# Optimization experiments

Hardware: AMD Instinct MI355X
Metric: run time of the kernel (lower is better)

## Reference

```python
import jax, jax.numpy as jnp
import numpy as np
from jax import lax

B, CIN, H, W = 64, 256, 56, 56
WIDTH = 64            # bottleneck width (planes * base_width/64 * groups)
COUT = 256            # planes * expansion
SP_BUDGET = 0.5       # spatial budget
CH_BUDGET = 0.5       # channel budget
K_SP = int(SP_BUDGET * H * W)    # 1568 kept pixels
K_CH = int(CH_BUDGET * WIDTH)    # 32 kept channels
EPS = 1e-5


def _conv(x, w, stride=1, pad=0):
    return lax.conv_general_dilated(
        x, w, (stride, stride), [(pad, pad), (pad, pad)],
        dimension_numbers=('NCHW', 'OIHW', 'NCHW'))


def _bn(x, g, b, m, v):
    scale = g / jnp.sqrt(v + EPS)
    return x * scale[None, :, None, None] + (b - m * scale)[None, :, None, None]


def setup_inputs() -> dict:
    key = jax.random.key(0)
    ks = jax.random.split(key, 6)
    inp = {
        'x': jax.random.normal(ks[0], (B, CIN, H, W), jnp.float32),
        'conv1_w': jax.random.normal(ks[1], (WIDTH, CIN, 1, 1), jnp.float32) * 0.05,
        'bn1_g': jnp.ones((WIDTH,), jnp.float32), 'bn1_b': jnp.zeros((WIDTH,), jnp.float32),
        'bn1_m': jnp.zeros((WIDTH,), jnp.float32), 'bn1_v': jnp.ones((WIDTH,), jnp.float32),
        'conv2_w': jax.random.normal(ks[2], (WIDTH, WIDTH, 3, 3), jnp.float32) * 0.05,
        'bn2_g': jnp.ones((WIDTH,), jnp.float32), 'bn2_b': jnp.zeros((WIDTH,), jnp.float32),
        'bn2_m': jnp.zeros((WIDTH,), jnp.float32), 'bn2_v': jnp.ones((WIDTH,), jnp.float32),
        'conv3_w': jax.random.normal(ks[3], (COUT, WIDTH, 1, 1), jnp.float32) * 0.05,
        'bn3_g': jnp.ones((COUT,), jnp.float32), 'bn3_b': jnp.zeros((COUT,), jnp.float32),
        'bn3_m': jnp.zeros((COUT,), jnp.float32), 'bn3_v': jnp.ones((COUT,), jnp.float32),
        'fc_w': jax.random.normal(ks[4], (WIDTH, CIN), jnp.float32) * 0.05,
        'fc_b': jnp.zeros((WIDTH,), jnp.float32),
        'mask_w': jax.random.normal(ks[5], (1, CIN, 1, 1), jnp.float32) * 0.05,
        'mask_b': jnp.zeros((1,), jnp.float32),
    }
    return inp


def reference(x, conv1_w, bn1_g, bn1_b, bn1_m, bn1_v,
              conv2_w, bn2_g, bn2_b, bn2_m, bn2_v,
              conv3_w, bn3_g, bn3_b, bn3_m, bn3_v,
              fc_w, fc_b, mask_w, mask_b):
    identity = x

    # --- ChannelVectorUnit: pooled fc saliency -> hard channel-budget top-k mask [B, WIDTH]
    pooled = x.mean(axis=(2, 3))                         # [B, CIN]
    ch_sal = jax.nn.sigmoid(pooled @ fc_w.T + fc_b)      # [B, WIDTH]
    ch_kth = lax.top_k(ch_sal, K_CH)[0][:, -1:]          # [B, 1]
    vector = (ch_sal >= ch_kth).astype(x.dtype)          # hard 0/1

    # --- MaskUnit: 1x1-conv spatial saliency -> hard spatial-budget top-k mask [B,1,H,W]
    sp_sal = _conv(x, mask_w) + mask_b[None, :, None, None]   # [B,1,H,W]
    sp_flat = sp_sal.reshape(B, H * W)
    sp_kth = lax.top_k(sp_flat, K_SP)[0][:, -1:]
    mask = (sp_flat >= sp_kth).astype(x.dtype).reshape(B, 1, H, W)
    # dilated mask: 3x3 max-dilation (receptive field of the 3x3 conv)
    mask_dilate = lax.reduce_window(mask, 0.0, lax.max, (1, 1, 3, 3), (1, 1, 1, 1), 'SAME')

    # --- masked bottleneck (dense compute, mask multiplies; stride = 1)
    out = _conv(x, conv1_w)
    out = jax.nn.relu(_bn(out, bn1_g, bn1_b, bn1_m, bn1_v)) * mask_dilate
    out = out * vector[:, :, None, None]                 # channel pruning
    out = _conv(out, conv2_w, stride=1, pad=1)
    out = jax.nn.relu(_bn(out, bn2_g, bn2_b, bn2_m, bn2_v)) * mask
    out = out * vector[:, :, None, None]
    out = _conv(out, conv3_w)
    out = _bn(out, bn3_g, bn3_b, bn3_m, bn3_v) * mask
    out = jax.nn.relu(identity + out)
    return out
```

## Files before the change

### kernel.cpp

```cpp
#include <hip/hip_runtime.h>
#include <math.h>

#define BATCH 64
#define CIN   256
#define HH    56
#define WW    56
#define HW    (HH*WW)
#define WIDTH 64
#define COUT  256
#define K_CH  32
#define K_SP  1568
#define EPS   1e-5f

typedef short short8 __attribute__((ext_vector_type(8)));
typedef float f32x4 __attribute__((ext_vector_type(4)));

#define MFMA16(a, b, c) __builtin_amdgcn_mfma_f32_16x16x32_bf16((a), (b), (c), 0, 0, 0)

__device__ __forceinline__ unsigned short f2bf(float f) {
    unsigned u = __builtin_bit_cast(unsigned, f);
    u += 0x7fffu + ((u >> 16) & 1u);
    return (unsigned short)(u >> 16);
}

__global__ __launch_bounds__(256) void k_poolsal(const float* __restrict__ x,
                                                 const float* __restrict__ mask_w,
                                                 double* __restrict__ pooled,
                                                 double* __restrict__ spart) {
    int ct = blockIdx.x, b = blockIdx.y;
    int tid = threadIdx.x;
    __shared__ double pl[16][257];
    double sp0[4], sp1[4], sp2[4], spt[4];
#pragma unroll
    for (int k = 0; k < 4; k++) { sp0[k] = 0.0; sp1[k] = 0.0; sp2[k] = 0.0; spt[k] = 0.0; }

#pragma clang loop unroll(disable)
    for (int c = 0; c < 16; c++) {
        const float* xr = x + ((size_t)(b * CIN + ct * 16 + c)) * HW;
        double w = (double)mask_w[ct * 16 + c];
        f32x4 v0 = *(const f32x4*)(xr + tid * 4);
        f32x4 v1 = *(const f32x4*)(xr + 1024 + tid * 4);
        f32x4 v2 = *(const f32x4*)(xr + 2048 + tid * 4);
        double s = 0.0;
#pragma unroll
        for (int k = 0; k < 4; k++) {
            double d0 = (double)v0[k], d1 = (double)v1[k], d2 = (double)v2[k];
            sp0[k] += d0 * w; sp1[k] += d1 * w; sp2[k] += d2 * w;
            s += d0 + d1 + d2;
        }
        if (tid < 16) {
            f32x4 v3 = *(const f32x4*)(xr + 3072 + tid * 4);
#pragma unroll
            for (int k = 0; k < 4; k++) {
                double d3 = (double)v3[k];
                spt[k] += d3 * w;
                s += d3;
            }
        }
        pl[c][tid] = s;
    }
    double* so = spart + ((size_t)(b * 16 + ct)) * HW;
#pragma unroll
    for (int k = 0; k < 4; k++) {
        so[tid * 4 + k] = sp0[k];
        so[1024 + tid * 4 + k] = sp1[k];
        so[2048 + tid * 4 + k] = sp2[k];
    }
    if (tid < 16) {
#pragma unroll
        for (int k = 0; k < 4; k++) so[3072 + tid * 4 + k] = spt[k];
    }
    __syncthreads();
    for (int off = 128; off > 0; off >>= 1) {
        for (int k = tid; k < 16 * off; k += 256) {
            int c = k / off, j = k - c * off;
            pl[c][j] += pl[c][j + off];
        }
        __syncthreads();
    }
    if (tid < 16) pooled[b * CIN + ct * 16 + tid] = pl[tid][0] * (1.0 / (double)HW);
}

__global__ __launch_bounds__(256) void k_sel(const double* __restrict__ pooled,
                                             const float* __restrict__ fc_w,
                                             const float* __restrict__ fc_b,
                                             const float* __restrict__ w2,
                                             const float* __restrict__ w3,
                                             const double* __restrict__ spart,
                                             float* __restrict__ vector,
                                             int* __restrict__ kidx,
                                             short* __restrict__ wt2c,
                                             short* __restrict__ w3c,
                                             float* __restrict__ mask,
                                             float* __restrict__ mdil) {
    int role = blockIdx.x >> 6;
    int b = blockIdx.x & 63;
    int tid = threadIdx.x;

    __shared__ unsigned long long ks[HW];
    __shared__ float m[HW];
    __shared__ unsigned int hist[256];
    __shared__ unsigned int sc[256];
    __shared__ unsigned long long sh_prefix;
    __shared__ unsigned int sh_krem;
    __shared__ double ps[CIN];
    __shared__ double ss[WIDTH];
    __shared__ double kth;
    __shared__ int ki[K_CH];

    if (role == 1) {
        for (int i = tid; i < CIN; i += 256) ps[i] = pooled[b * CIN + i];
        __syncthreads();
        if (tid < 64) {
            double acc = (double)fc_b[tid];
            const float* wr = fc_w + tid * CIN;
            for (int k = 0; k < CIN; k++) acc += ps[k] * (double)wr[k];
            ss[tid] = 1.0 / (1.0 + exp(-acc));
        }
        __syncthreads();
        if (tid < 64) {
            double sal = ss[tid];
            int cg = 0, ce = 0;
            for (int i = 0; i < WIDTH; i++) {
                cg += (ss[i] > sal);
                ce += (ss[i] == sal);
            }
            if (cg <= K_CH - 1 && cg + ce >= K_CH) kth = sal;
        }
        __syncthreads();
        if (tid < 64) {
            double sal = ss[tid];
            int kept = (sal >= kth) ? 1 : 0;
            vector[b * WIDTH + tid] = (float)kept;
            int pos = 0;
            for (int i = 0; i < tid; i++) pos += (ss[i] >= kth) ? 1 : 0;
            if (kept && pos < K_CH) { kidx[b * K_CH + pos] = tid; ki[pos] = tid; }
        }
        __syncthreads();
        for (int i = tid; i < 9216; i += 256) {
            int tap = i >> 10, rem = i & 1023;
            int oc_c = rem >> 5, c_c = rem & 31;
            wt2c[(size_t)b * 9216 + i] = (short)f2bf(w2[ki[oc_c] * 576 + ki[c_c] * 9 + tap]);
        }
        for (int i = tid; i < 8192; i += 256) {
            int oc = i >> 5, c_c = i & 31;
            w3c[(size_t)b * 8192 + i] = (short)f2bf(w3[oc * 64 + ki[c_c]]);
        }
        return;
    }

#pragma unroll
    for (int i = 0; i < 13; i++) {
        int px = i * 256 + tid;
        if (px < HW) {
            double s = 0.0;
#pragma unroll
            for (int t = 0; t < 16; t++) s += spart[((size_t)(b * 16 + t)) * HW + px];
            unsigned long long u = __builtin_bit_cast(unsigned long long, s);
            ks[px] = (u >> 63) ? ~u : (u | 0x8000000000000000ULL);
        }
    }
    if (tid == 0) { sh_prefix = 0ULL; sh_krem = K_SP; }
    __syncthreads();

    unsigned long long pmask = 0ULL;
    for (int pass = 0; pass < 8; pass++) {
        int shift = 56 - 8 * pass;
        hist[tid] = 0;
        __syncthreads();
        unsigned long long prefix = sh_prefix;
#pragma unroll
        for (int i = 0; i < 13; i++) {
            int px = i * 256 + tid;
            if (px < HW) {
                unsigned long long k = ks[px];
                if ((k & pmask) == prefix)
                    atomicAdd(&hist[(unsigned)((k >> shift) & 255ULL)], 1u);
            }
        }
        __syncthreads();
        sc[tid] = hist[255 - tid];
        __syncthreads();
        for (int off = 1; off < 256; off <<= 1) {
            unsigned v = sc[tid];
            unsigned a = (tid >= off) ? sc[tid - off] : 0u;
            __syncthreads();
            sc[tid] = v + a;
            __syncthreads();
        }
        unsigned krem = sh_krem;
        unsigned cum = sc[tid];
        unsigned cumHigher = (tid > 0) ? sc[tid - 1] : 0u;
        __syncthreads();
        if (cum >= krem && cumHigher < krem) {
            int d = 255 - tid;
            sh_krem = krem - cumHigher;
            sh_prefix = prefix | ((unsigned long long)d << shift);
        }
        pmask |= (0xFFULL << shift);
        __syncthreads();
    }
    unsigned long long kthk = sh_prefix;

#pragma unroll
    for (int i = 0; i < 13; i++) {
        int px = i * 256 + tid;
        if (px < HW) {
            float mv = (ks[px] >= kthk) ? 1.0f : 0.0f;
            m[px] = mv;
            mask[b * HW + px] = mv;
        }
    }
    __syncthreads();
    for (int p = tid; p < HW; p += 256) {
        int y = p / WW, xx = p % WW;
        float mx = 0.0f;
        for (int dy = -1; dy <= 1; dy++) {
            int yy = y + dy;
            if (yy < 0 || yy >= HH) continue;
            for (int dx = -1; dx <= 1; dx++) {
                int xc = xx + dx;
                if (xc < 0 || xc >= WW) continue;
                mx = fmaxf(mx, m[yy * WW + xc]);
            }
        }
        mdil[b * HW + p] = mx;
    }
}

__global__ __launch_bounds__(256, 2) void k_conv1(const float* __restrict__ x,
                                                  const float* __restrict__ w1,
                                                  const float* __restrict__ g1, const float* __restrict__ b1,
                                                  const float* __restrict__ m1, const float* __restrict__ v1,
                                                  const float* __restrict__ mdil,
                                                  const int* __restrict__ kidx,
                                                  short* __restrict__ out1c) {
    __shared__ float scc[32], shc[32];
    __shared__ int ki[32];
    int b = blockIdx.y, p0 = blockIdx.x * 448;
    int tid = threadIdx.x, w = tid >> 6, lane = tid & 63, g = lane >> 4, ln = lane & 15;
    if (tid < 32) {
        int c = kidx[b * K_CH + tid];
        ki[tid] = c;
        float s = g1[c] * rsqrtf(v1[c] + EPS);
        scc[tid] = s; shc[tid] = b1[c] - m1[c] * s;
    }
    __syncthreads();

    int pxw = p0 + w * 112 + ln;
    f32x4 acc[2][7];
    f32x4 zz = {0.f, 0.f, 0.f, 0.f};
#pragma unroll
    for (int m = 0; m < 2; m++)
#pragma unroll
        for (int nt = 0; nt < 7; nt++) acc[m][nt] = zz;

#pragma unroll
    for (int ks = 0; ks < 8; ks++) {
        short8 afr[2];
#pragma unroll
        for (int m = 0; m < 2; m++) {
            const float* wp = w1 + (ki[m * 16 + ln] * 256 + ks * 32 + g * 8);
            f32x4 a0 = *(const f32x4*)(wp);
            f32x4 a1 = *(const f32x4*)(wp + 4);
#pragma unroll
            for (int j = 0; j < 4; j++) {
                afr[m][j]     = (short)f2bf(a0[j]);
                afr[m][4 + j] = (short)f2bf(a1[j]);
            }
        }
        const float* xp0 = x + ((size_t)(b * 256 + ks * 32 + g * 8)) * HW + pxw;
#pragma unroll
        for (int nt = 0; nt < 7; nt++) {
            const float* xp = xp0 + nt * 16;
            short8 bfr;
#pragma unroll
            for (int j = 0; j < 8; j++)
                bfr[j] = (short)f2bf(xp[(size_t)j * HW]);
#pragma unroll
            for (int m = 0; m < 2; m++) acc[m][nt] = MFMA16(afr[m], bfr, acc[m][nt]);
        }
    }
#pragma unroll
    for (int nt = 0; nt < 7; nt++) {
        int px = pxw + nt * 16;
        float md = mdil[b * HW + px];
#pragma unroll
        for (int m = 0; m < 2; m++) {
            int oc = m * 16 + g * 4;
            float y0 = fmaxf(acc[m][nt][0] * scc[oc + 0] + shc[oc + 0], 0.f) * md;
            float y1 = fmaxf(acc[m][nt][1] * scc[oc + 1] + shc[oc + 1], 0.f) * md;
            float y2 = fmaxf(acc[m][nt][2] * scc[oc + 2] + shc[oc + 2], 0.f) * md;
            float y3 = fmaxf(acc[m][nt][3] * scc[oc + 3] + shc[oc + 3], 0.f) * md;
            uint2 u;
            u.x = (unsigned)f2bf(y0) | ((unsigned)f2bf(y1) << 16);
            u.y = (unsigned)f2bf(y2) | ((unsigned)f2bf(y3) << 16);
            *(uint2*)(out1c + ((size_t)(b * HW + px)) * 32 + oc) = u;
        }
    }
}

__global__ __launch_bounds__(128, 2) void k_conv2(const short* __restrict__ out1c,
                                                  const short* __restrict__ wt2c,
                                                  const float* __restrict__ g2, const float* __restrict__ b2,
                                                  const float* __restrict__ m2, const float* __restrict__ v2,
                                                  const float* __restrict__ mask,
                                                  const int* __restrict__ kidx,
                                                  short* __restrict__ out2c) {
    __shared__ short lds[6 * 58 * 32];
    __shared__ float scc[32], shc[32];
    int b = blockIdx.y, r0 = blockIdx.x * 4, p0 = r0 * 56;
    int tid = threadIdx.x, w = tid >> 6, lane = tid & 63, g = lane >> 4, ln = lane & 15;
    if (tid < 32) {
        int c = kidx[b * K_CH + tid];
        float s = g2[c] * rsqrtf(v2[c] + EPS);
        scc[tid] = s; shc[tid] = b2[c] - m2[c] * s;
    }
    short8 z8 = {0, 0, 0, 0, 0, 0, 0, 0};
    for (int i = tid; i < 1392; i += 128) {
        int cblk = i & 3;
        int colr = i >> 2;
        int col = colr % 58, ri = colr / 58;
        int gr = r0 - 1 + ri, gc = col - 1;
        short8 v8 = z8;
        if (gr >= 0 && gr < HH && gc >= 0 && gc < WW)
            v8 = *(const short8*)(out1c + ((size_t)(b * HW + gr * WW + gc)) * 32 + cblk * 8);
        *(short8*)(&lds[(ri * 58 + col) * 32 + ((cblk * 8) ^ ((col & 3) << 3))]) = v8;
    }
    __syncthreads();

    f32x4 acc[2][7];
    f32x4 zz = {0.f, 0.f, 0.f, 0.f};
#pragma unroll
    for (int m = 0; m < 2; m++)
#pragma unroll
        for (int nt = 0; nt < 7; nt++) acc[m][nt] = zz;

    const short* wtb = wt2c + (size_t)b * 9216;
    int prel0 = w * 112 + ln;
    for (int tap = 0; tap < 9; tap++) {
        int dy = tap / 3 - 1;
        int dx = tap - (tap / 3) * 3 - 1;
        short8 afr[2];
#pragma unroll
        for (int m = 0; m < 2; m++)
            afr[m] = *(const short8*)(wtb + tap * 1024 + (m * 16 + ln) * 32 + g * 8);
#pragma unroll
        for (int nt = 0; nt < 7; nt++) {
            int prel = prel0 + nt * 16;
            int rrel = prel / 56;
            int xcol = prel - rrel * 56;
            int row_l = rrel + 1 + dy;
            int col_l = xcol + 1 + dx;
            short8 bfr = *(const short8*)(&lds[(row_l * 58 + col_l) * 32 + ((g * 8) ^ ((col_l & 3) << 3))]);
#pragma unroll
            for (int m = 0; m < 2; m++) acc[m][nt] = MFMA16(afr[m], bfr, acc[m][nt]);
        }
    }
#pragma unroll
    for (int nt = 0; nt < 7; nt++) {
        int px = p0 + prel0 + nt * 16;
        float mv = mask[b * HW + px];
#pragma unroll
        for (int m = 0; m < 2; m++) {
            int oc = m * 16 + g * 4;
            float y0 = fmaxf(acc[m][nt][0] * scc[oc + 0] + shc[oc + 0], 0.f) * mv;
            float y1 = fmaxf(acc[m][nt][1] * scc[oc + 1] + shc[oc + 1], 0.f) * mv;
            float y2 = fmaxf(acc[m][nt][2] * scc[oc + 2] + shc[oc + 2], 0.f) * mv;
            float y3 = fmaxf(acc[m][nt][3] * scc[oc + 3] + shc[oc + 3], 0.f) * mv;
            uint2 u;
            u.x = (unsigned)f2bf(y0) | ((unsigned)f2bf(y1) << 16);
            u.y = (unsigned)f2bf(y2) | ((unsigned)f2bf(y3) << 16);
            *(uint2*)(out2c + ((size_t)(b * HW + px)) * 32 + oc) = u;
        }
    }
}

__global__ __launch_bounds__(256, 4) void k_conv3(const short* __restrict__ out2c,
                                                  const short* __restrict__ w3c,
                                                  const float* __restrict__ g3, const float* __restrict__ b3,
                                                  const float* __restrict__ m3, const float* __restrict__ v3,
                                                  const float* __restrict__ mask,
                                                  const float* __restrict__ x,
                                                  float* __restrict__ out) {
    int b = blockIdx.y;
    int ocb = blockIdx.x / 28;
    int pxb = blockIdx.x % 28;
    int p0 = pxb * 112;
    int tid = threadIdx.x, w = tid >> 6, lane = tid & 63, g = lane >> 4, ln = lane & 15;
    int oc0 = ocb * 64 + w * 16;
    int oc = oc0 + ln;

    const short* w3b = w3c + (size_t)b * 8192;
    short8 wfr = *(const short8*)(w3b + oc * 32 + g * 8);

    short8 act[7];
#pragma unroll
    for (int nt = 0; nt < 7; nt++)
        act[nt] = *(const short8*)(out2c + ((size_t)(b * HW + p0 + nt * 16 + ln)) * 32 + g * 8);

    f32x4 xr[7];
#pragma unroll
    for (int nt = 0; nt < 7; nt++) {
        int px0 = p0 + nt * 16 + g * 4;
        xr[nt] = *(const f32x4*)(x + ((size_t)(b * COUT + oc)) * HW + px0);
    }
    __builtin_amdgcn_sched_barrier(0);

    f32x4 acc[7];
    f32x4 zz = {0.f, 0.f, 0.f, 0.f};
#pragma unroll
    for (int nt = 0; nt < 7; nt++) acc[nt] = zz;
#pragma unroll
    for (int nt = 0; nt < 7; nt++)
        acc[nt] = MFMA16(act[nt], wfr, acc[nt]);

    float s_ = g3[oc] * rsqrtf(v3[oc] + EPS);
    float h_ = b3[oc] - m3[oc] * s_;
#pragma unroll
    for (int nt = 0; nt < 7; nt++) {
        int px0 = p0 + nt * 16 + g * 4;
        f32x4 mv = *(const f32x4*)(mask + (size_t)b * HW + px0);
        size_t idx = ((size_t)(b * COUT + oc)) * HW + px0;
        f32x4 o;
#pragma unroll
        for (int i = 0; i < 4; i++)
            o[i] = fmaxf(xr[nt][i] + (acc[nt][i] * s_ + h_) * mv[i], 0.f);
        *(f32x4*)(out + idx) = o;
    }
}

extern "C" void kernel_launch(void* const* d_in, const int* in_sizes, int n_in,
                              void* d_out, int out_size, void* d_ws, size_t ws_size,
                              hipStream_t stream) {
    const float* x       = (const float*)d_in[0];
    const float* conv1_w = (const float*)d_in[1];
    const float* bn1_g   = (const float*)d_in[2];
    const float* bn1_b   = (const float*)d_in[3];
    const float* bn1_m   = (const float*)d_in[4];
    const float* bn1_v   = (const float*)d_in[5];
    const float* conv2_w = (const float*)d_in[6];
    const float* bn2_g   = (const float*)d_in[7];
    const float* bn2_b   = (const float*)d_in[8];
    const float* bn2_m   = (const float*)d_in[9];
    const float* bn2_v   = (const float*)d_in[10];
    const float* conv3_w = (const float*)d_in[11];
    const float* bn3_g   = (const float*)d_in[12];
    const float* bn3_b   = (const float*)d_in[13];
    const float* bn3_m   = (const float*)d_in[14];
    const float* bn3_v   = (const float*)d_in[15];
    const float* fc_w    = (const float*)d_in[16];
    const float* fc_b    = (const float*)d_in[17];
    const float* mask_w  = (const float*)d_in[18];
    const float* mask_b  = (const float*)d_in[19];
    (void)mask_b;

    char* wsb = (char*)d_ws;
    size_t off = 0;
    double* pooled = (double*)(wsb + off); off += (size_t)BATCH * CIN * 8;
    double* spart  = (double*)(wsb + off); off += (size_t)BATCH * 16 * HW * 8;
    float* vector  = (float*)(wsb + off);  off += (size_t)BATCH * WIDTH * 4;
    float* mask    = (float*)(wsb + off);  off += (size_t)BATCH * HW * 4;
    float* mdil    = (float*)(wsb + off);  off += (size_t)BATCH * HW * 4;
    int*   kidx    = (int*)(wsb + off);    off += (size_t)BATCH * K_CH * 4;
    short* wt2c    = (short*)(wsb + off);  off += (size_t)BATCH * 9216 * 2;
    short* w3c     = (short*)(wsb + off);  off += (size_t)BATCH * 8192 * 2;
    short* out1c   = (short*)(wsb + off);  off += (size_t)BATCH * HW * 32 * 2;
    short* out2c   = (short*)(wsb + off);  off += (size_t)BATCH * HW * 32 * 2;
    (void)ws_size; (void)in_sizes; (void)n_in; (void)out_size; (void)vector;

    k_poolsal<<<dim3(16, BATCH), 256, 0, stream>>>(x, mask_w, pooled, spart);
    k_sel<<<128, 256, 0, stream>>>(pooled, fc_w, fc_b, conv2_w, conv3_w, spart,
                                   vector, kidx, wt2c, w3c, mask, mdil);
    k_conv1<<<dim3(7, BATCH), 256, 0, stream>>>(x, conv1_w, bn1_g, bn1_b, bn1_m, bn1_v, mdil, kidx, out1c);
    k_conv2<<<dim3(14, BATCH), 128, 0, stream>>>(out1c, wt2c, bn2_g, bn2_b, bn2_m, bn2_v, mask, kidx, out2c);
    k_conv3<<<dim3(112, BATCH), 256, 0, stream>>>(out2c, w3c, bn3_g, bn3_b, bn3_m, bn3_v, mask, x, (float*)d_out);
}
```

Baseline: 215.4 us.

## Fuse pooling and spatial saliency into conv1, computing all 64 channels before selection

The separate pooling/saliency pass over x is merged into conv1, so x (205 MB fp32) is read once instead of twice. Because the channel selection is not known yet, conv1 now computes all 64 output channels and stores a 64-channel bf16 intermediate. The spatial dilation mask and channel mask are applied when conv2 loads its tile, and conv2 contracts over all 64 input channels. This trades extra MFMA work, a doubled intermediate size and doubled conv2 K-dimension for removing one full read of x and a kernel launch.

Result: slower. 235.4 us (+9.3%).

```diff
diff --git a/kernel.cpp b/kernel.cpp
--- a/kernel.cpp
+++ b/kernel.cpp
@@ -23,72 +23,127 @@
     return (unsigned short)(u >> 16);
 }
 
-__global__ __launch_bounds__(256) void k_poolsal(const float* __restrict__ x,
-                                                 const float* __restrict__ mask_w,
-                                                 double* __restrict__ pooled,
-                                                 double* __restrict__ spart) {
-    int ct = blockIdx.x, b = blockIdx.y;
-    int tid = threadIdx.x;
-    __shared__ double pl[16][257];
-    double sp0[4], sp1[4], sp2[4], spt[4];
-#pragma unroll
-    for (int k = 0; k < 4; k++) { sp0[k] = 0.0; sp1[k] = 0.0; sp2[k] = 0.0; spt[k] = 0.0; }
+__global__ __launch_bounds__(256, 2) void k_fused1(const float* __restrict__ x,
+                                                   const float* __restrict__ w1,
+                                                   const float* __restrict__ g1, const float* __restrict__ b1,
+                                                   const float* __restrict__ m1, const float* __restrict__ v1,
+                                                   const float* __restrict__ mask_w,
+                                                   short* __restrict__ out1h,
+                                                   double* __restrict__ spsal,
+                                                   double* __restrict__ pooled_part) {
+    __shared__ float scc[64], shc[64];
+    __shared__ float wsh[256];
+    __shared__ double pl[32][65];
+    int b = blockIdx.y, chunk = blockIdx.x, p0 = chunk * 448;
+    int tid = threadIdx.x, w = tid >> 6, lane = tid & 63, g = lane >> 4, ln = lane & 15;
+    if (tid < 64) {
+        float s = g1[tid] * rsqrtf(v1[tid] + EPS);
+        scc[tid] = s; shc[tid] = b1[tid] - m1[tid] * s;
+    }
+    wsh[tid] = mask_w[tid];
+    __syncthreads();
+
+    int pxw = p0 + w * 112 + ln;
+    f32x4 acc[4][7];
+    f32x4 zz = {0.f, 0.f, 0.f, 0.f};
+#pragma unroll
+    for (int m = 0; m < 4; m++)
+#pragma unroll
+        for (int nt = 0; nt < 7; nt++) acc[m][nt] = zz;
+    double sp[7];
+#pragma unroll
+    for (int nt = 0; nt < 7; nt++) sp[nt] = 0.0;
 
 #pragma clang loop unroll(disable)
-    for (int c = 0; c < 16; c++) {
-        const float* xr = x + ((size_t)(b * CIN + ct * 16 + c)) * HW;
-        double w = (double)mask_w[ct * 16 + c];
-        f32x4 v0 = *(const f32x4*)(xr + tid * 4);
-        f32x4 v1 = *(const f32x4*)(xr + 1024 + tid * 4);
-        f32x4 v2 = *(const f32x4*)(xr + 2048 + tid * 4);
-        double s = 0.0;
-#pragma unroll
-        for (int k = 0; k < 4; k++) {
-            double d0 = (double)v0[k], d1 = (double)v1[k], d2 = (double)v2[k];
-            sp0[k] += d0 * w; sp1[k] += d1 * w; sp2[k] += d2 * w;
-            s += d0 + d1 + d2;
-        }
-        if (tid < 16) {
-            f32x4 v3 = *(const f32x4*)(xr + 3072 + tid * 4);
-#pragma unroll
-            for (int k = 0; k < 4; k++) {
-                double d3 = (double)v3[k];
-                spt[k] += d3 * w;
-                s += d3;
-            }
-        }
-        pl[c][tid] = s;
-    }
-    double* so = spart + ((size_t)(b * 16 + ct)) * HW;
-#pragma unroll
-    for (int k = 0; k < 4; k++) {
-        so[tid * 4 + k] = sp0[k];
-        so[1024 + tid * 4 + k] = sp1[k];
-        so[2048 + tid * 4 + k] = sp2[k];
-    }
-    if (tid < 16) {
-#pragma unroll
-        for (int k = 0; k < 4; k++) so[3072 + tid * 4 + k] = spt[k];
-    }
-    __syncthreads();
-    for (int off = 128; off > 0; off >>= 1) {
-        for (int k = tid; k < 16 * off; k += 256) {
-            int c = k / off, j = k - c * off;
-            pl[c][j] += pl[c][j + off];
-        }
-        __syncthreads();
-    }
-    if (tid < 16) pooled[b * CIN + ct * 16 + tid] = pl[tid][0] * (1.0 / (double)HW);
-}
-
-__global__ __launch_bounds__(256) void k_sel(const double* __restrict__ pooled,
+    for (int ks = 0; ks < 8; ks++) {
+        short8 afr[4];
+#pragma unroll
+        for (int m = 0; m < 4; m++) {
+            const float* wp = w1 + ((m * 16 + ln) * 256 + ks * 32 + g * 8);
+            f32x4 a0 = *(const f32x4*)(wp);
+            f32x4 a1 = *(const f32x4*)(wp + 4);
+#pragma unroll
+            for (int j = 0; j < 4; j++) {
+                afr[m][j]     = (short)f2bf(a0[j]);
+                afr[m][4 + j] = (short)f2bf(a1[j]);
+            }
+        }
+        float wc[8];
+#pragma unroll
+        for (int j = 0; j < 8; j++) wc[j] = wsh[ks * 32 + g * 8 + j];
+        double pc[8];
+#pragma unroll
+        for (int j = 0; j < 8; j++) pc[j] = 0.0;
+
+        const float* xp0 = x + ((size_t)(b * 256 + ks * 32 + g * 8)) * HW + pxw;
+#pragma unroll
+        for (int nt = 0; nt < 7; nt++) {
+            const float* xp = xp0 + nt * 16;
+            float xv[8];
+#pragma unroll
+            for (int j = 0; j < 8; j++) xv[j] = xp[(size_t)j * HW];
+            short8 bfr;
+            double s = 0.0;
+#pragma unroll
+            for (int j = 0; j < 8; j++) {
+                bfr[j] = (short)f2bf(xv[j]);
+                double d = (double)xv[j];
+                s += d * (double)wc[j];
+                pc[j] += d;
+            }
+            sp[nt] += s;
+#pragma unroll
+            for (int m = 0; m < 4; m++) acc[m][nt] = MFMA16(afr[m], bfr, acc[m][nt]);
+        }
+        __syncthreads();
+#pragma unroll
+        for (int j = 0; j < 8; j++) pl[g * 8 + j][w * 16 + ln] = pc[j];
+        __syncthreads();
+        for (int off = 32; off > 0; off >>= 1) {
+            for (int k2 = tid; k2 < 32 * off; k2 += 256) {
+                int ch = k2 / off, i2 = k2 - ch * off;
+                pl[ch][i2] += pl[ch][i2 + off];
+            }
+            __syncthreads();
+        }
+        if (tid < 32)
+            pooled_part[((size_t)(b * 7 + chunk)) * 256 + ks * 32 + tid] = pl[tid][0];
+    }
+
+#pragma unroll
+    for (int nt = 0; nt < 7; nt++) {
+        double s = sp[nt];
+        s += __shfl_xor(s, 16, 64);
+        s += __shfl_xor(s, 32, 64);
+        if (g == 0) spsal[(size_t)b * HW + pxw + nt * 16] = s;
+    }
+
+#pragma unroll
+    for (int nt = 0; nt < 7; nt++) {
+        int px = pxw + nt * 16;
+#pragma unroll
+        for (int m = 0; m < 4; m++) {
+            int oc = m * 16 + g * 4;
+            float y0 = fmaxf(acc[m][nt][0] * scc[oc + 0] + shc[oc + 0], 0.f);
+            float y1 = fmaxf(acc[m][nt][1] * scc[oc + 1] + shc[oc + 1], 0.f);
+            float y2 = fmaxf(acc[m][nt][2] * scc[oc + 2] + shc[oc + 2], 0.f);
+            float y3 = fmaxf(acc[m][nt][3] * scc[oc + 3] + shc[oc + 3], 0.f);
+            uint2 u;
+            u.x = (unsigned)f2bf(y0) | ((unsigned)f2bf(y1) << 16);
+            u.y = (unsigned)f2bf(y2) | ((unsigned)f2bf(y3) << 16);
+            *(uint2*)(out1h + ((size_t)(b * HW + px)) * 64 + m * 16 + g * 4) = u;
+        }
+    }
+}
+
+__global__ __launch_bounds__(256) void k_sel(const double* __restrict__ pooled_part,
                                              const float* __restrict__ fc_w,
                                              const float* __restrict__ fc_b,
                                              const float* __restrict__ w2,
                                              const float* __restrict__ w3,
-                                             const double* __restrict__ spart,
-                                             float* __restrict__ vector,
+                                             const double* __restrict__ spsal,
                                              int* __restrict__ kidx,
+                                             unsigned short* __restrict__ kmask,
                                              short* __restrict__ wt2c,
                                              short* __restrict__ w3c,
                                              float* __restrict__ mask,
@@ -109,7 +164,11 @@
     __shared__ int ki[K_CH];
 
     if (role == 1) {
-        for (int i = tid; i < CIN; i += 256) ps[i] = pooled[b * CIN + i];
+        for (int i = tid; i < CIN; i += 256) {
+            double s = 0.0;
+            for (int k = 0; k < 7; k++) s += pooled_part[((size_t)(b * 7 + k)) * 256 + i];
+            ps[i] = s * (1.0 / (double)HW);
+        }
         __syncthreads();
         if (tid < 64) {
             double acc = (double)fc_b[tid];
@@ -131,16 +190,16 @@
         if (tid < 64) {
             double sal = ss[tid];
             int kept = (sal >= kth) ? 1 : 0;
-            vector[b * WIDTH + tid] = (float)kept;
+            kmask[b * WIDTH + tid] = kept ? 0xFFFFu : 0u;
             int pos = 0;
             for (int i = 0; i < tid; i++) pos += (ss[i] >= kth) ? 1 : 0;
             if (kept && pos < K_CH) { kidx[b * K_CH + pos] = tid; ki[pos] = tid; }
         }
         __syncthreads();
-        for (int i = tid; i < 9216; i += 256) {
-            int tap = i >> 10, rem = i & 1023;
-            int oc_c = rem >> 5, c_c = rem & 31;
-            wt2c[(size_t)b * 9216 + i] = (short)f2bf(w2[ki[oc_c] * 576 + ki[c_c] * 9 + tap]);
+        for (int i = tid; i < 18432; i += 256) {
+            int tap = i >> 11, rem = i & 2047;
+            int oc_c = rem >> 6, c = rem & 63;
+            wt2c[(size_t)b * 18432 + i] = (short)f2bf(w2[ki[oc_c] * 576 + c * 9 + tap]);
         }
         for (int i = tid; i < 8192; i += 256) {
             int oc = i >> 5, c_c = i & 31;
@@ -153,9 +212,7 @@
     for (int i = 0; i < 13; i++) {
         int px = i * 256 + tid;
         if (px < HW) {
-            double s = 0.0;
-#pragma unroll
-            for (int t = 0; t < 16; t++) s += spart[((size_t)(b * 16 + t)) * HW + px];
+            double s = spsal[(size_t)b * HW + px];
             unsigned long long u = __builtin_bit_cast(unsigned long long, s);
             ks[px] = (u >> 63) ? ~u : (u | 0x8000000000000000ULL);
         }
@@ -228,87 +285,18 @@
     }
 }
 
-__global__ __launch_bounds__(256, 2) void k_conv1(const float* __restrict__ x,
-                                                  const float* __restrict__ w1,
-                                                  const float* __restrict__ g1, const float* __restrict__ b1,
-                                                  const float* __restrict__ m1, const float* __restrict__ v1,
-                                                  const float* __restrict__ mdil,
-                                                  const int* __restrict__ kidx,
-                                                  short* __restrict__ out1c) {
-    __shared__ float scc[32], shc[32];
-    __shared__ int ki[32];
-    int b = blockIdx.y, p0 = blockIdx.x * 448;
-    int tid = threadIdx.x, w = tid >> 6, lane = tid & 63, g = lane >> 4, ln = lane & 15;
-    if (tid < 32) {
-        int c = kidx[b * K_CH + tid];
-        ki[tid] = c;
-        float s = g1[c] * rsqrtf(v1[c] + EPS);
-        scc[tid] = s; shc[tid] = b1[c] - m1[c] * s;
-    }
-    __syncthreads();
-
-    int pxw = p0 + w * 112 + ln;
-    f32x4 acc[2][7];
-    f32x4 zz = {0.f, 0.f, 0.f, 0.f};
-#pragma unroll
-    for (int m = 0; m < 2; m++)
-#pragma unroll
-        for (int nt = 0; nt < 7; nt++) acc[m][nt] = zz;
-
-#pragma unroll
-    for (int ks = 0; ks < 8; ks++) {
-        short8 afr[2];
-#pragma unroll
-        for (int m = 0; m < 2; m++) {
-            const float* wp = w1 + (ki[m * 16 + ln] * 256 + ks * 32 + g * 8);
-            f32x4 a0 = *(const f32x4*)(wp);
-            f32x4 a1 = *(const f32x4*)(wp + 4);
-#pragma unroll
-            for (int j = 0; j < 4; j++) {
-                afr[m][j]     = (short)f2bf(a0[j]);
-                afr[m][4 + j] = (short)f2bf(a1[j]);
-            }
-        }
-        const float* xp0 = x + ((size_t)(b * 256 + ks * 32 + g * 8)) * HW + pxw;
-#pragma unroll
-        for (int nt = 0; nt < 7; nt++) {
-            const float* xp = xp0 + nt * 16;
-            short8 bfr;
-#pragma unroll
-            for (int j = 0; j < 8; j++)
-                bfr[j] = (short)f2bf(xp[(size_t)j * HW]);
-#pragma unroll
-            for (int m = 0; m < 2; m++) acc[m][nt] = MFMA16(afr[m], bfr, acc[m][nt]);
-        }
-    }
-#pragma unroll
-    for (int nt = 0; nt < 7; nt++) {
-        int px = pxw + nt * 16;
-        float md = mdil[b * HW + px];
-#pragma unroll
-        for (int m = 0; m < 2; m++) {
-            int oc = m * 16 + g * 4;
-            float y0 = fmaxf(acc[m][nt][0] * scc[oc + 0] + shc[oc + 0], 0.f) * md;
-            float y1 = fmaxf(acc[m][nt][1] * scc[oc + 1] + shc[oc + 1], 0.f) * md;
-            float y2 = fmaxf(acc[m][nt][2] * scc[oc + 2] + shc[oc + 2], 0.f) * md;
-            float y3 = fmaxf(acc[m][nt][3] * scc[oc + 3] + shc[oc + 3], 0.f) * md;
-            uint2 u;
-            u.x = (unsigned)f2bf(y0) | ((unsigned)f2bf(y1) << 16);
-            u.y = (unsigned)f2bf(y2) | ((unsigned)f2bf(y3) << 16);
-            *(uint2*)(out1c + ((size_t)(b * HW + px)) * 32 + oc) = u;
-        }
-    }
-}
-
-__global__ __launch_bounds__(128, 2) void k_conv2(const short* __restrict__ out1c,
+__global__ __launch_bounds__(128, 2) void k_conv2(const short* __restrict__ out1h,
                                                   const short* __restrict__ wt2c,
                                                   const float* __restrict__ g2, const float* __restrict__ b2,
                                                   const float* __restrict__ m2, const float* __restrict__ v2,
                                                   const float* __restrict__ mask,
+                                                  const float* __restrict__ mdil,
                                                   const int* __restrict__ kidx,
+                                                  const unsigned short* __restrict__ kmask,
                                                   short* __restrict__ out2c) {
-    __shared__ short lds[6 * 58 * 32];
+    __shared__ short lds[6 * 58 * 64];
     __shared__ float scc[32], shc[32];
+    __shared__ unsigned short kms[64];
     int b = blockIdx.y, r0 = blockIdx.x * 4, p0 = r0 * 56;
     int tid = threadIdx.x, w = tid >> 6, lane = tid & 63, g = lane >> 4, ln = lane & 15;
     if (tid < 32) {
@@ -316,16 +304,25 @@
         float s = g2[c] * rsqrtf(v2[c] + EPS);
         scc[tid] = s; shc[tid] = b2[c] - m2[c] * s;
     }
+    if (tid < 64) kms[tid] = kmask[b * WIDTH + tid];
+    __syncthreads();
     short8 z8 = {0, 0, 0, 0, 0, 0, 0, 0};
-    for (int i = tid; i < 1392; i += 128) {
-        int cblk = i & 3;
-        int colr = i >> 2;
+    for (int i = tid; i < 2784; i += 128) {
+        int cblk = i & 7;
+        int colr = i >> 3;
         int col = colr % 58, ri = colr / 58;
         int gr = r0 - 1 + ri, gc = col - 1;
         short8 v8 = z8;
-        if (gr >= 0 && gr < HH && gc >= 0 && gc < WW)
-            v8 = *(const short8*)(out1c + ((size_t)(b * HW + gr * WW + gc)) * 32 + cblk * 8);
-        *(short8*)(&lds[(ri * 58 + col) * 32 + ((cblk * 8) ^ ((col & 3) << 3))]) = v8;
+        if (gr >= 0 && gr < HH && gc >= 0 && gc < WW) {
+            int gpx = b * HW + gr * WW + gc;
+            v8 = *(const short8*)(out1h + ((size_t)gpx) * 64 + cblk * 8);
+            unsigned short mm = (mdil[gpx] != 0.0f) ? 0xFFFFu : 0u;
+            short8 km = *(const short8*)(&kms[cblk * 8]);
+#pragma unroll
+            for (int j = 0; j < 8; j++)
+                v8[j] = (short)(v8[j] & km[j] & (short)mm);
+        }
+        *(short8*)(&lds[(ri * 58 + col) * 64 + ((cblk * 8) ^ ((col & 7) << 3))]) = v8;
     }
     __syncthreads();
 
@@ -336,15 +333,17 @@
 #pragma unroll
         for (int nt = 0; nt < 7; nt++) acc[m][nt] = zz;
 
-    const short* wtb = wt2c + (size_t)b * 9216;
+    const short* wtb = wt2c + (size_t)b * 18432;
     int prel0 = w * 112 + ln;
     for (int tap = 0; tap < 9; tap++) {
         int dy = tap / 3 - 1;
         int dx = tap - (tap / 3) * 3 - 1;
-        short8 afr[2];
+        short8 afr[2][2];
 #pragma unroll
         for (int m = 0; m < 2; m++)
-            afr[m] = *(const short8*)(wtb + tap * 1024 + (m * 16 + ln) * 32 + g * 8);
+#pragma unroll
+            for (int ks2 = 0; ks2 < 2; ks2++)
+                afr[m][ks2] = *(const short8*)(wtb + tap * 2048 + (m * 16 + ln) * 64 + ks2 * 32 + g * 8);
 #pragma unroll
         for (int nt = 0; nt < 7; nt++) {
             int prel = prel0 + nt * 16;
@@ -352,9 +351,14 @@
             int xcol = prel - rrel * 56;
             int row_l = rrel + 1 + dy;
             int col_l = xcol + 1 + dx;
-            short8 bfr = *(const short8*)(&lds[(row_l * 58 + col_l) * 32 + ((g * 8) ^ ((col_l & 3) << 3))]);
-#pragma unroll
-            for (int m = 0; m < 2; m++) acc[m][nt] = MFMA16(afr[m], bfr, acc[m][nt]);
+            int base = (row_l * 58 + col_l) * 64;
+            int sw = (col_l & 7) << 3;
+#pragma unroll
+            for (int ks2 = 0; ks2 < 2; ks2++) {
+                short8 bfr = *(const short8*)(&lds[base + ((ks2 * 32 + g * 8) ^ sw)]);
+#pragma unroll
+                for (int m = 0; m < 2; m++) acc[m][nt] = MFMA16(afr[m][ks2], bfr, acc[m][nt]);
+            }
         }
     }
 #pragma unroll
@@ -457,22 +461,23 @@
 
     char* wsb = (char*)d_ws;
     size_t off = 0;
-    double* pooled = (double*)(wsb + off); off += (size_t)BATCH * CIN * 8;
-    double* spart  = (double*)(wsb + off); off += (size_t)BATCH * 16 * HW * 8;
-    float* vector  = (float*)(wsb + off);  off += (size_t)BATCH * WIDTH * 4;
+    double* pooled_part = (double*)(wsb + off); off += (size_t)BATCH * 7 * 256 * 8;
+    double* spsal  = (double*)(wsb + off); off += (size_t)BATCH * HW * 8;
     float* mask    = (float*)(wsb + off);  off += (size_t)BATCH * HW * 4;
     float* mdil    = (float*)(wsb + off);  off += (size_t)BATCH * HW * 4;
     int*   kidx    = (int*)(wsb + off);    off += (size_t)BATCH * K_CH * 4;
-    short* wt2c    = (short*)(wsb + off);  off += (size_t)BATCH * 9216 * 2;
+    unsigned short* kmask = (unsigned short*)(wsb + off); off += (size_t)BATCH * WIDTH * 2;
+    short* wt2c    = (short*)(wsb + off);  off += (size_t)BATCH * 18432 * 2;
     short* w3c     = (short*)(wsb + off);  off += (size_t)BATCH * 8192 * 2;
-    short* out1c   = (short*)(wsb + off);  off += (size_t)BATCH * HW * 32 * 2;
+    short* out1h   = (short*)(wsb + off);  off += (size_t)BATCH * HW * 64 * 2;
     short* out2c   = (short*)(wsb + off);  off += (size_t)BATCH * HW * 32 * 2;
-    (void)ws_size; (void)in_sizes; (void)n_in; (void)out_size; (void)vector;
-
-    k_poolsal<<<dim3(16, BATCH), 256, 0, stream>>>(x, mask_w, pooled, spart);
-    k_sel<<<128, 256, 0, stream>>>(pooled, fc_w, fc_b, conv2_w, conv3_w, spart,
-                                   vector, kidx, wt2c, w3c, mask, mdil);
-    k_conv1<<<dim3(7, BATCH), 256, 0, stream>>>(x, conv1_w, bn1_g, bn1_b, bn1_m, bn1_v, mdil, kidx, out1c);
-    k_conv2<<<dim3(14, BATCH), 128, 0, stream>>>(out1c, wt2c, bn2_g, bn2_b, bn2_m, bn2_v, mask, kidx, out2c);
+    (void)ws_size; (void)in_sizes; (void)n_in; (void)out_size;
+
+    k_fused1<<<dim3(7, BATCH), 256, 0, stream>>>(x, conv1_w, bn1_g, bn1_b, bn1_m, bn1_v,
+                                                 mask_w, out1h, spsal, pooled_part);
+    k_sel<<<128, 256, 0, stream>>>(pooled_part, fc_w, fc_b, conv2_w, conv3_w, spsal,
+                                   kidx, kmask, wt2c, w3c, mask, mdil);
+    k_conv2<<<dim3(14, BATCH), 128, 0, stream>>>(out1h, wt2c, bn2_g, bn2_b, bn2_m, bn2_v,
+                                                 mask, mdil, kidx, kmask, out2c);
     k_conv3<<<dim3(112, BATCH), 256, 0, stream>>>(out2c, w3c, bn3_g, bn3_b, bn3_m, bn3_v, mask, x, (float*)d_out);
 }
```
